# Kernel tuning notes

Hardware: AMD Instinct MI355X
Metric: run time of the kernel (lower is better)

The kernel has to match this reference:

```python
import jax, jax.numpy as jnp
import numpy as np

B, T, L, D, H, E, A, V = 64, 20, 196, 512, 512, 512, 512, 30000


def setup_inputs() -> dict:
    key = jax.random.key(0)
    ks = jax.random.split(key, 20)
    s = 0.02  # param init scale
    inp = {
        "captions": jax.random.randint(ks[0], (B, T), 0, V),
        "image_features": jax.random.normal(ks[1], (B, L, D), dtype=jnp.float32),
        "pooled_features": jax.random.normal(ks[2], (B, H), dtype=jnp.float32),
        "attention_mask": jnp.ones((B, L), dtype=bool),
        # embedding table
        "embedding": jax.random.normal(ks[3], (V, E), dtype=jnp.float32) * s,
        # LSTM (torch gate order i, f, g, o), input = [emb; context]
        "W_ih": jax.random.normal(ks[4], (4 * H, E + H), dtype=jnp.float32) * s,
        "W_hh": jax.random.normal(ks[5], (4 * H, H), dtype=jnp.float32) * s,
        "b_lstm": jnp.zeros((4 * H,), dtype=jnp.float32),
        # additive attention with memory/cell extra query context
        "Wq": jax.random.normal(ks[6], (H, A), dtype=jnp.float32) * s,
        "Wk": jax.random.normal(ks[7], (D, A), dtype=jnp.float32) * s,
        "Wm": jax.random.normal(ks[8], (H, A), dtype=jnp.float32) * s,
        "Wc": jax.random.normal(ks[9], (H, A), dtype=jnp.float32) * s,
        "v_att": jax.random.normal(ks[10], (A,), dtype=jnp.float32) * s,
        # output projection context(H) -> vocab
        "W_out": jax.random.normal(ks[11], (H, V), dtype=jnp.float32) * s,
        "b_out": jnp.zeros((V,), dtype=jnp.float32),
        # hidden/cell init from pooled features (num_layers = 1)
        "W_init_h": jax.random.normal(ks[12], (H, H), dtype=jnp.float32) * s,
        "b_init_h": jnp.zeros((H,), dtype=jnp.float32),
        "W_init_c": jax.random.normal(ks[13], (H, H), dtype=jnp.float32) * s,
        "b_init_c": jnp.zeros((H,), dtype=jnp.float32),
    }
    return inp


def reference(captions, image_features, pooled_features, attention_mask,
              embedding, W_ih, W_hh, b_lstm, Wq, Wk, Wm, Wc, v_att,
              W_out, b_out, W_init_h, b_init_h, W_init_c, b_init_c):
    # init hidden states from pooled features
    h0 = pooled_features @ W_init_h + b_init_h            # [B, H]
    c0 = pooled_features @ W_init_c + b_init_c            # [B, H]
    ctx0 = jnp.zeros_like(h0)                              # prev_context, [B, H]
    emb = embedding[captions]                              # [B, T, E] (dropout = eval identity)
    # precompute key projection once (hoisted out of the timestep loop)
    key_proj = jnp.einsum('bld,da->bla', image_features, Wk)  # [B, L, A]
    neg = jnp.finfo(image_features.dtype).min

    def step(carry, emb_t):
        h, c, ctx = carry
        x = jnp.concatenate([emb_t, ctx], axis=-1)         # [B, E+H]
        gates = x @ W_ih.T + h @ W_hh.T + b_lstm           # [B, 4H]
        i, f, g, o = jnp.split(gates, 4, axis=-1)
        i = jax.nn.sigmoid(i); f = jax.nn.sigmoid(f)
        g = jnp.tanh(g);       o = jax.nn.sigmoid(o)
        c_new = f * c + i * g
        h_new = o * jnp.tanh(c_new)                        # lstm output == query
        # additive attention: query + memory_state(h) + cell_state(c) context
        q = h_new @ Wq + h_new @ Wm + c_new @ Wc           # [B, A]
        scores = jnp.einsum('bla,a->bl', jnp.tanh(key_proj + q[:, None, :]), v_att)
        scores = jnp.where(attention_mask, scores, neg)
        w = jax.nn.softmax(scores, axis=-1)                # [B, L]
        ctx_new = jnp.einsum('bl,bld->bd', w, image_features)  # [B, H]
        logits_t = ctx_new @ W_out + b_out                 # [B, V]
        return (h_new, c_new, ctx_new), logits_t

    _, logits = jax.lax.scan(step, (h0, c0, ctx0), jnp.swapaxes(emb, 0, 1))
    return jnp.swapaxes(logits, 0, 1)  # [B, T, V]
```

## Files before the change

kernel.cpp:

```cpp
#include <hip/hip_runtime.h>
#include <hip/hip_bf16.h>
#include <cstdint>

#define DEV static __device__ __forceinline__

typedef __bf16 bf16;
typedef __bf16 bf16x8 __attribute__((ext_vector_type(8)));
typedef float f32x4 __attribute__((ext_vector_type(4)));

#define B_ 64
#define T_ 20
#define L_ 196
#define E_ 512
#define V_ 30000
#define VPAD 30080
#define XK 2560
#define GN 2048
#define KSPLIT 8
#define KSPAN 10

DEV float sigmoidf_(float x) { return 1.0f / (1.0f + __expf(-x)); }
DEV float tanhf_(float x) { float e = __expf(2.0f * x); return 1.0f - 2.0f / (e + 1.0f); }

DEV float ldf(const void* p, size_t i, int isbf) {
  return isbf ? (float)((const bf16*)p)[i] : ((const float*)p)[i];
}

DEV void gload_lds16(const void* g, void* l) {
  __builtin_amdgcn_global_load_lds(
      (const __attribute__((address_space(1))) void*)(uintptr_t)g,
      (__attribute__((address_space(3))) void*)(uint32_t)(uintptr_t)l,
      16, 0, 0);
}

__global__ void k_detect(const void* __restrict__ emb, int* __restrict__ flag)
{
  if (threadIdx.x == 0) {
    const unsigned* w = (const unsigned*)emb;
    int cnt = 0;
    for (int i = 0; i < 256; ++i) {
      unsigned lo = w[i] & 0xFFFFu;
      unsigned e = (lo >> 7) & 0xFFu;
      if (e >= 100 && e <= 126) ++cnt;
    }
    *flag = (cnt >= 128) ? 1 : 0;
  }
}

__global__ __launch_bounds__(256)
void k_init_mm(const void* __restrict__ pooled, const void* __restrict__ W_init_h,
               const void* __restrict__ W_init_c, float* __restrict__ ipart,
               const int* __restrict__ flag)
{
  const int isbf = *flag;
  const int b = blockIdx.x, ks = blockIdx.y, mat = blockIdx.z;
  const void* W = mat ? W_init_c : W_init_h;
  const int tid = threadIdx.x;
  __shared__ float p_s[64];
  if (tid < 64) p_s[tid] = ldf(pooled, (size_t)b * 512 + ks * 64 + tid, isbf);
  __syncthreads();
  const int kb = ks * 64;
  float a0 = 0.0f, a1 = 0.0f;
#pragma unroll 8
  for (int k = 0; k < 64; ++k) {
    float p = p_s[k];
    a0 += p * ldf(W, (size_t)(kb + k) * 512 + tid, isbf);
    a1 += p * ldf(W, (size_t)(kb + k) * 512 + tid + 256, isbf);
  }
  float* o = ipart + (((size_t)mat * 8 + ks) * 64 + b) * 512;
  o[tid] = a0;
  o[tid + 256] = a1;
}

__global__ __launch_bounds__(256)
void k_pack(const float* __restrict__ ipart, const void* __restrict__ b_init_h,
            const void* __restrict__ b_init_c, const int* __restrict__ captions,
            const void* __restrict__ embedding, const void* __restrict__ Wq,
            const void* __restrict__ Wm, const void* __restrict__ Wc,
            bf16* __restrict__ xcomb, float* __restrict__ c_state,
            bf16* __restrict__ Wqm, bf16* __restrict__ Wcb,
            const int* __restrict__ flag)
{
  const int isbf = *flag;
  const int tid = threadIdx.x;
  if (blockIdx.x >= 96) {
    size_t base = (size_t)(blockIdx.x - 96) * 8192;
    for (int i = tid; i < 8192; i += 256)
      Wcb[base + i] = (bf16)ldf(Wc, base + i, isbf);
    return;
  }
  if (blockIdx.x >= 64) {
    size_t base = (size_t)(blockIdx.x - 64) * 8192;
    for (int i = tid; i < 8192; i += 256)
      Wqm[base + i] = (bf16)(ldf(Wq, base + i, isbf) + ldf(Wm, base + i, isbf));
    return;
  }
  const int b = blockIdx.x;
  {
    int cap = captions[b * T_];
    for (int i = tid; i < 512; i += 256) {
      xcomb[(size_t)b * XK + i] = (bf16)ldf(embedding, (size_t)cap * E_ + i, isbf);
      xcomb[(size_t)b * XK + 512 + i]  = (bf16)0.0f;
      xcomb[(size_t)b * XK + 1024 + i] = (bf16)0.0f;
    }
  }
#pragma unroll
  for (int jj = 0; jj < 2; ++jj) {
    int j = tid + jj * 256;
    float ah = ldf(b_init_h, j, isbf), ac = ldf(b_init_c, j, isbf);
#pragma unroll
    for (int ks = 0; ks < 8; ++ks) {
      ah += ipart[(((size_t)0 * 8 + ks) * 64 + b) * 512 + j];
      ac += ipart[(((size_t)1 * 8 + ks) * 64 + b) * 512 + j];
    }
    c_state[b * 512 + j] = ac;
    bf16 hh = (bf16)ah;
    xcomb[(size_t)b * XK + 1536 + j] = hh;
    xcomb[(size_t)b * XK + 2048 + j] = (bf16)(ah - (float)hh);
  }
}

__global__ __launch_bounds__(256)
void k_gemm(const void* __restrict__ A, const void* __restrict__ Bsrc,
            int N, int K, int kspan, int outmode, int amode, int btmode,
            float* __restrict__ outF, bf16* __restrict__ outB,
            void* __restrict__ outAny, const void* __restrict__ bias,
            const int* __restrict__ flag)
{
  const int isbf = *flag;
  const int tid  = threadIdx.x;
  const int lane = tid & 63, w = tid >> 6;
  const int n0 = blockIdx.x * 64;
  const int yt = blockIdx.y;
  const int m0 = (outmode == 1) ? 0 : yt * 64;
  const int kbase = (outmode == 1) ? yt * kspan * 32 : 0;

  __shared__ __align__(16) bf16 As[64 * 32];
  __shared__ __align__(16) bf16 Bs[64 * 32];

  f32x4 acc[2][2];
#pragma unroll
  for (int i = 0; i < 2; ++i)
#pragma unroll
    for (int j = 0; j < 2; ++j)
#pragma unroll
      for (int r = 0; r < 4; ++r) acc[i][j][r] = 0.0f;

  const int wm = (w & 1) * 32, wn = (w >> 1) * 32;
  const int sr = tid >> 2, sk = (tid & 3) * 8;
  const int fm = lane & 15, kq = (lane >> 4) * 8;
  const bool bvalid = (n0 + sr) < N;
  const int kk = tid >> 3, nn = (tid & 7) * 8;

  for (int ks = 0; ks < kspan; ++ks) {
    const size_t aidx = (size_t)(m0 + sr) * K + kbase + sk + ks * 32;
    bf16x8 av;
    if (amode == 0 || isbf) {
      av = *(const bf16x8*)((const bf16*)A + aidx);
    } else {
      const float* af = (const float*)A + aidx;
      float4 x0 = *(const float4*)af, x1 = *(const float4*)(af + 4);
      av[0] = (bf16)x0.x; av[1] = (bf16)x0.y; av[2] = (bf16)x0.z; av[3] = (bf16)x0.w;
      av[4] = (bf16)x1.x; av[5] = (bf16)x1.y; av[6] = (bf16)x1.z; av[7] = (bf16)x1.w;
    }

    if (btmode == 0) {
      bf16x8 bv;
#pragma unroll
      for (int i = 0; i < 8; ++i) bv[i] = (bf16)0.0f;
      if (bvalid)
        bv = *(const bf16x8*)((const bf16*)Bsrc + (size_t)(n0 + sr) * K + kbase + sk + ks * 32);
      __syncthreads();
      *(bf16x8*)(As + sr * 32 + sk) = av;
      *(bf16x8*)(Bs + sr * 32 + sk) = bv;
      __syncthreads();
    } else {
      float bl[8];
      const int krow = kbase + ks * 32 + kk;
#pragma unroll
      for (int i = 0; i < 8; ++i) {
        int n = n0 + nn + i;
        bl[i] = (n < N) ? ldf(Bsrc, (size_t)krow * N + n, isbf) : 0.0f;
      }
      __syncthreads();
      *(bf16x8*)(As + sr * 32 + sk) = av;
#pragma unroll
      for (int i = 0; i < 8; ++i) Bs[(nn + i) * 32 + kk] = (bf16)bl[i];
      __syncthreads();
    }

    bf16x8 a0 = *(const bf16x8*)(As + (wm + fm)      * 32 + kq);
    bf16x8 a1 = *(const bf16x8*)(As + (wm + 16 + fm) * 32 + kq);
    bf16x8 b0 = *(const bf16x8*)(Bs + (wn + fm)      * 32 + kq);
    bf16x8 b1 = *(const bf16x8*)(Bs + (wn + 16 + fm) * 32 + kq);
    acc[0][0] = __builtin_amdgcn_mfma_f32_16x16x32_bf16(a0, b0, acc[0][0], 0, 0, 0);
    acc[0][1] = __builtin_amdgcn_mfma_f32_16x16x32_bf16(a0, b1, acc[0][1], 0, 0, 0);
    acc[1][0] = __builtin_amdgcn_mfma_f32_16x16x32_bf16(a1, b0, acc[1][0], 0, 0, 0);
    acc[1][1] = __builtin_amdgcn_mfma_f32_16x16x32_bf16(a1, b1, acc[1][1], 0, 0, 0);
  }

  const int rbase = (lane >> 4) * 4;
  if (outmode == 1) {
    float* o = outF + (size_t)yt * 64 * N;
#pragma unroll
    for (int i = 0; i < 2; ++i)
#pragma unroll
      for (int j = 0; j < 2; ++j)
#pragma unroll
        for (int r = 0; r < 4; ++r) {
          int m = wm + i * 16 + rbase + r;
          int n = n0 + wn + j * 16 + fm;
          o[(size_t)m * N + n] = acc[i][j][r];
        }
  } else if (outmode == 0) {
#pragma unroll
    for (int i = 0; i < 2; ++i)
#pragma unroll
      for (int j = 0; j < 2; ++j) {
        int n = n0 + wn + j * 16 + fm;
        if (n < N) {
#pragma unroll
          for (int r = 0; r < 4; ++r) {
            int m = m0 + wm + i * 16 + rbase + r;
            outB[(size_t)m * N + n] = (bf16)acc[i][j][r];
          }
        }
      }
  } else {
#pragma unroll
    for (int i = 0; i < 2; ++i)
#pragma unroll
      for (int j = 0; j < 2; ++j) {
        int n = n0 + wn + j * 16 + fm;
        if (n < N) {
          float bb = bias ? ldf(bias, n, isbf) : 0.0f;
#pragma unroll
          for (int r = 0; r < 4; ++r) {
            int m = m0 + wm + i * 16 + rbase + r;
            float val = acc[i][j][r] + bb;
            if (isbf) ((bf16*)outAny)[(size_t)m * N + n] = (bf16)val;
            else      ((float*)outAny)[(size_t)m * N + n] = val;
          }
        }
      }
  }
}

__global__ __launch_bounds__(256)
void k_gemm128(const bf16* __restrict__ A, const bf16* __restrict__ BT,
               int N, int K,
               void* __restrict__ outAny, const void* __restrict__ bias,
               const int* __restrict__ flag)
{
  const int isbf = *flag;
  const int tid = threadIdx.x, lane = tid & 63, w = tid >> 6;

  const int NMT = (B_ * T_) / 128;
  const int nwg = (int)gridDim.x * (int)gridDim.y;
  const int wgid = (int)blockIdx.y * (int)gridDim.x + (int)blockIdx.x;
  const int xcd = wgid & 7, loc = wgid >> 3;
  const int qq = nwg >> 3, rr = nwg & 7;
  const int swz = (xcd < rr ? xcd * (qq + 1) : rr * (qq + 1) + (xcd - rr) * qq) + loc;
  const int n0 = (swz / NMT) * 128, m0 = (swz % NMT) * 128;

  __shared__ __align__(16) bf16 As[128 * 32];
  __shared__ __align__(16) bf16 Bs[128 * 32];

  f32x4 acc[4][4];
#pragma unroll
  for (int i = 0; i < 4; ++i)
#pragma unroll
    for (int j = 0; j < 4; ++j)
#pragma unroll
      for (int r = 0; r < 4; ++r) acc[i][j][r] = 0.0f;

  const int lr = lane >> 2;
  const int lk = (lane & 3) * 8;
  const int fm = lane & 15, kq = (lane >> 4) * 8;
  const int wm = (w & 1) * 64, wn = (w >> 1) * 64;
  const int li0 = w * 2, li1 = w * 2 + 1;

  const bf16* a0g = A  + (size_t)(m0 + li0 * 16 + lr) * K + lk;
  const bf16* a1g = A  + (size_t)(m0 + li1 * 16 + lr) * K + lk;
  const bf16* b0g = BT + (size_t)(n0 + li0 * 16 + lr) * K + lk;
  const bf16* b1g = BT + (size_t)(n0 + li1 * 16 + lr) * K + lk;

  const int kiters = K >> 5;
  for (int ks = 0; ks < kiters; ++ks) {
    const int k0 = ks * 32;
    gload_lds16(a0g + k0, As + li0 * 512);
    gload_lds16(a1g + k0, As + li1 * 512);
    gload_lds16(b0g + k0, Bs + li0 * 512);
    gload_lds16(b1g + k0, Bs + li1 * 512);
    __syncthreads();
    bf16x8 af[4], bf[4];
#pragma unroll
    for (int i = 0; i < 4; ++i) {
      af[i] = *(const bf16x8*)(As + (wm + i * 16 + fm) * 32 + kq);
      bf[i] = *(const bf16x8*)(Bs + (wn + i * 16 + fm) * 32 + kq);
    }
#pragma unroll
    for (int i = 0; i < 4; ++i)
#pragma unroll
      for (int j = 0; j < 4; ++j)
        acc[i][j] = __builtin_amdgcn_mfma_f32_16x16x32_bf16(af[i], bf[j], acc[i][j], 0, 0, 0);
    __syncthreads();
  }

  const int rbase = (lane >> 4) * 4;
#pragma unroll
  for (int j = 0; j < 4; ++j) {
    int n = n0 + wn + j * 16 + fm;
    if (n < N) {
      float bb = bias ? ldf(bias, n, isbf) : 0.0f;
#pragma unroll
      for (int i = 0; i < 4; ++i)
#pragma unroll
        for (int r = 0; r < 4; ++r) {
          int m = m0 + wm + i * 16 + rbase + r;
          float val = acc[i][j][r] + bb;
          if (isbf) ((bf16*)outAny)[(size_t)m * N + n] = (bf16)val;
          else      ((float*)outAny)[(size_t)m * N + n] = val;
        }
    }
  }
}

__global__ __launch_bounds__(256)
void k_transpose(const void* __restrict__ in, bf16* __restrict__ out, int R, int C,
                 int Cpad, const int* __restrict__ flag)
{
  const int isbf = *flag;
  __shared__ bf16 tile[32][33];
  const int c0 = blockIdx.x * 32, r0 = blockIdx.y * 32;
  const int cc = threadIdx.x & 31, rw = threadIdx.x >> 5;
#pragma unroll
  for (int s = 0; s < 4; ++s) {
    int r = r0 + rw + s * 8, c = c0 + cc;
    tile[rw + s * 8][cc] = (r < R && c < C) ? (bf16)ldf(in, (size_t)r * C + c, isbf)
                                            : (bf16)0.0f;
  }
  __syncthreads();
#pragma unroll
  for (int s = 0; s < 4; ++s) {
    int c = c0 + rw + s * 8, r = r0 + cc;
    if (c < Cpad && r < R) out[(size_t)c * R + r] = tile[cc][rw + s * 8];
  }
}

__global__ __launch_bounds__(256)
void k_buildWcomb(const void* __restrict__ W_ih, const void* __restrict__ W_hh,
                  bf16* __restrict__ WcombT, const int* __restrict__ flag)
{
  const int isbf = *flag;
  const int n = blockIdx.x;
  for (int k = threadIdx.x; k < XK; k += 256) {
    float v;
    if (k < 512)       v = ldf(W_ih, (size_t)n * 1024 + k, isbf);
    else if (k < 1536) v = ldf(W_ih, (size_t)n * 1024 + 512 + ((k - 512) & 511), isbf);
    else               v = ldf(W_hh, (size_t)n * 512 + ((k - 1536) & 511), isbf);
    WcombT[(size_t)n * XK + k] = (bf16)v;
  }
}

__global__ __launch_bounds__(1024)
void k_step2(const float* __restrict__ partials, const void* __restrict__ b_lstm,
             float* __restrict__ c_state, bf16* __restrict__ xcomb,
             bf16* __restrict__ ctx_all, const bf16* __restrict__ Wqm,
             const bf16* __restrict__ Wcb, const bf16* __restrict__ keyproj,
             const void* __restrict__ v_att, const void* __restrict__ img,
             const int* __restrict__ captions, const void* __restrict__ embedding,
             int t, const int* __restrict__ flag)
{
  const int isbf = *flag;
  const int b = blockIdx.x, tid = threadIdx.x;
  __shared__ float h_s[512], c_s[512], q_s[512];
  __shared__ float red[16 * 512];
  __shared__ float sc_s[256];
  __shared__ float wred[32];

#pragma unroll
  for (int jj = 0; jj < 2; ++jj) {
    int gc = tid + jj * 1024;
    float s = ldf(b_lstm, gc, isbf);
#pragma unroll
    for (int sp = 0; sp < KSPLIT; ++sp)
      s += partials[((size_t)sp * 64 + b) * 2048 + gc];
    red[gc] = s;
  }
  __syncthreads();
  if (tid < 512) {
    const int j = tid;
    float ig = sigmoidf_(red[j]);
    float fg = sigmoidf_(red[512 + j]);
    float gg = tanhf_(red[1024 + j]);
    float og = sigmoidf_(red[1536 + j]);
    float cn = fg * c_state[b * 512 + j] + ig * gg;
    float hn = og * tanhf_(cn);
    c_state[b * 512 + j] = cn;
    h_s[j] = hn; c_s[j] = cn;
    bf16 hh = (bf16)hn;
    xcomb[(size_t)b * XK + 1536 + j] = hh;
    xcomb[(size_t)b * XK + 2048 + j] = (bf16)(hn - (float)hh);
  }
  __syncthreads();

  {
    const int dc = tid >> 6, a8 = (tid & 63) * 8;
    float qp[8];
#pragma unroll
    for (int i = 0; i < 8; ++i) qp[i] = 0.0f;
    const int d0 = dc * 32;
    for (int d = d0; d < d0 + 32; ++d) {
      float hv = h_s[d], cv = c_s[d];
      bf16x8 wq = *(const bf16x8*)(Wqm + (size_t)d * 512 + a8);
      bf16x8 wc = *(const bf16x8*)(Wcb + (size_t)d * 512 + a8);
#pragma unroll
      for (int i = 0; i < 8; ++i)
        qp[i] += hv * (float)wq[i] + cv * (float)wc[i];
    }
#pragma unroll
    for (int i = 0; i < 8; ++i) red[dc * 512 + a8 + i] = qp[i];
  }
  __syncthreads();
  if (tid < 512) {
    float s = 0.0f;
#pragma unroll
    for (int w16 = 0; w16 < 16; ++w16) s += red[w16 * 512 + tid];
    q_s[tid] = s;
  }
  __syncthreads();

  {
    const int wv = tid >> 6, ln = tid & 63;
    float q8[8], v8[8];
#pragma unroll
    for (int i = 0; i < 8; ++i) {
      q8[i] = q_s[ln * 8 + i];
      v8[i] = ldf(v_att, ln * 8 + i, isbf);
    }
    for (int l = wv; l < 196; l += 16) {
      bf16x8 kv = *(const bf16x8*)(keyproj + ((size_t)b * 196 + l) * 512 + ln * 8);
      float s = 0.0f;
#pragma unroll
      for (int i = 0; i < 8; ++i)
        s += tanhf_((float)kv[i] + q8[i]) * v8[i];
      s += __shfl_xor(s, 32); s += __shfl_xor(s, 16); s += __shfl_xor(s, 8);
      s += __shfl_xor(s, 4);  s += __shfl_xor(s, 2);  s += __shfl_xor(s, 1);
      if (ln == 0) sc_s[l] = s;
    }
  }
  __syncthreads();

  {
    const int wv = tid >> 6, ln = tid & 63;
    float v = (tid < 196) ? sc_s[tid] : -3.0e38f;
    float m = v;
    m = fmaxf(m, __shfl_xor(m, 32)); m = fmaxf(m, __shfl_xor(m, 16));
    m = fmaxf(m, __shfl_xor(m, 8));  m = fmaxf(m, __shfl_xor(m, 4));
    m = fmaxf(m, __shfl_xor(m, 2));  m = fmaxf(m, __shfl_xor(m, 1));
    if (ln == 0) wred[wv] = m;
    __syncthreads();
    m = wred[0];
#pragma unroll
    for (int i = 1; i < 16; ++i) m = fmaxf(m, wred[i]);
    float e = (tid < 196) ? __expf(v - m) : 0.0f;
    float ss = e;
    ss += __shfl_xor(ss, 32); ss += __shfl_xor(ss, 16); ss += __shfl_xor(ss, 8);
    ss += __shfl_xor(ss, 4);  ss += __shfl_xor(ss, 2);  ss += __shfl_xor(ss, 1);
    if (ln == 0) wred[16 + wv] = ss;
    __syncthreads();
    float tot = 0.0f;
#pragma unroll
    for (int i = 0; i < 16; ++i) tot += wred[16 + i];
    if (tid < 196) sc_s[tid] = e / tot;
  }
  __syncthreads();

  {
    const int d8 = (tid & 63) * 8, lc = tid >> 6;
    float cx[8];
#pragma unroll
    for (int i = 0; i < 8; ++i) cx[i] = 0.0f;
    if (isbf) {
      for (int l = lc; l < 196; l += 16) {
        float wl = sc_s[l];
        bf16x8 iv = *(const bf16x8*)((const bf16*)img + ((size_t)b * 196 + l) * 512 + d8);
#pragma unroll
        for (int i = 0; i < 8; ++i) cx[i] += wl * (float)iv[i];
      }
    } else {
      for (int l = lc; l < 196; l += 16) {
        float wl = sc_s[l];
        const float* ip = (const float*)img + ((size_t)b * 196 + l) * 512 + d8;
        float4 x0 = *(const float4*)ip, x1 = *(const float4*)(ip + 4);
        cx[0] += wl * x0.x; cx[1] += wl * x0.y; cx[2] += wl * x0.z; cx[3] += wl * x0.w;
        cx[4] += wl * x1.x; cx[5] += wl * x1.y; cx[6] += wl * x1.z; cx[7] += wl * x1.w;
      }
    }
#pragma unroll
    for (int i = 0; i < 8; ++i) red[lc * 512 + d8 + i] = cx[i];
  }
  __syncthreads();
  if (tid < 512) {
    const int d = tid;
    float s = 0.0f;
#pragma unroll
    for (int w16 = 0; w16 < 16; ++w16) s += red[w16 * 512 + d];
    bf16 ch = (bf16)s;
    xcomb[(size_t)b * XK + 512 + d]  = ch;
    xcomb[(size_t)b * XK + 1024 + d] = (bf16)(s - (float)ch);
    ctx_all[((size_t)b * T_ + t) * 512 + d] = ch;
  }
  if (t + 1 < T_) {
    int cap = captions[b * T_ + t + 1];
    for (int i = tid; i < 512; i += 1024)
      xcomb[(size_t)b * XK + i] = (bf16)ldf(embedding, (size_t)cap * E_ + i, isbf);
  }
}

extern "C" void kernel_launch(void* const* d_in, const int* in_sizes, int n_in,
                              void* d_out, int out_size, void* d_ws, size_t ws_size,
                              hipStream_t stream)
{
  (void)in_sizes; (void)n_in; (void)out_size;
  const int*  captions  = (const int*)d_in[0];
  const void* img       = d_in[1];
  const void* pooled    = d_in[2];
  const void* embedding = d_in[4];
  const void* W_ih      = d_in[5];
  const void* W_hh      = d_in[6];
  const void* b_lstm    = d_in[7];
  const void* Wq        = d_in[8];
  const void* Wk        = d_in[9];
  const void* Wm        = d_in[10];
  const void* Wc        = d_in[11];
  const void* v_att     = d_in[12];
  const void* W_out     = d_in[13];
  const void* b_out     = d_in[14];
  const void* W_init_h  = d_in[15];
  const void* b_init_h  = d_in[16];
  const void* W_init_c  = d_in[17];
  const void* b_init_c  = d_in[18];

  char* ws = (char*)d_ws;
  size_t off = 0;
  auto alloc = [&](size_t bytes) {
    void* p = ws + off;
    off += (bytes + 255) & ~(size_t)255;
    return p;
  };
  int*   flag     = (int*)alloc(256);
  bf16*  xcomb    = (bf16*)alloc((size_t)B_ * XK * 2);
  float* c_state  = (float*)alloc((size_t)B_ * 512 * 4);
  bf16*  ctx_all  = (bf16*)alloc((size_t)B_ * T_ * 512 * 2);
  bf16*  Wqm      = (bf16*)alloc((size_t)512 * 512 * 2);
  bf16*  Wcb      = (bf16*)alloc((size_t)512 * 512 * 2);
  bf16*  WkT      = (bf16*)alloc((size_t)512 * 512 * 2);
  float* partials = (float*)alloc((size_t)KSPLIT * B_ * GN * 4);
  bf16*  keyproj  = (bf16*)alloc((size_t)B_ * L_ * 512 * 2);
  bf16*  WcombT   = (bf16*)alloc((size_t)GN * XK * 2);
  bf16*  WoutT    = (bf16*)alloc((size_t)VPAD * 512 * 2);
  const bool fits = (off <= ws_size);
  float* ipart = partials;

  k_detect<<<1, 64, 0, stream>>>(embedding, flag);
  k_init_mm<<<dim3(64, 8, 2), 256, 0, stream>>>(pooled, W_init_h, W_init_c, ipart, flag);
  k_pack<<<128, 256, 0, stream>>>(ipart, b_init_h, b_init_c, captions, embedding,
                                  Wq, Wm, Wc, xcomb, c_state, Wqm, Wcb, flag);
  k_buildWcomb<<<GN, 256, 0, stream>>>(W_ih, W_hh, WcombT, flag);
  k_transpose<<<dim3(16, 16), 256, 0, stream>>>(Wk, WkT, 512, 512, 512, flag);
  if (fits)
    k_transpose<<<dim3(VPAD / 32, 16), 256, 0, stream>>>(W_out, WoutT, 512, V_, VPAD, flag);

  k_gemm<<<dim3(8, L_ * B_ / 64), 256, 0, stream>>>(
      img, WkT, 512, 512, 16, 0, 1, 0,
      nullptr, keyproj, nullptr, nullptr, flag);

  for (int t = 0; t < T_; ++t) {
    k_gemm<<<dim3(GN / 64, KSPLIT), 256, 0, stream>>>(
        xcomb, WcombT, GN, XK, KSPAN, 1, 0, 0,
        partials, nullptr, nullptr, nullptr, flag);
    k_step2<<<B_, 1024, 0, stream>>>(partials, b_lstm, c_state, xcomb, ctx_all,
                                     Wqm, Wcb, keyproj, v_att, img, captions,
                                     embedding, t, flag);
  }

  if (fits) {
    k_gemm128<<<dim3(VPAD / 128, B_ * T_ / 128), 256, 0, stream>>>(
        ctx_all, WoutT, V_, 512, d_out, b_out, flag);
  } else {
    k_gemm<<<dim3((V_ + 63) / 64, B_ * T_ / 64), 256, 0, stream>>>(
        ctx_all, W_out, V_, 512, 16, 2, 0, 1,
        nullptr, nullptr, d_out, b_out, flag);
  }
}
```

Measured before the change: 1.393 ms.

## Double-buffer LDS loads in gate and vocab GEMMs with a dedicated gates kernel

Adds a specialized k_gates kernel for the per-step LSTM gate GEMM. It double-buffers global-to-LDS loads and uses manual vmcnt waits and barriers, so the next K-slice is fetched while MFMAs run on the current one. k_gemm128 (the vocab projection) gets the same two-stage LDS pipeline, which doubles its shared-memory use. The aim is to hide global load latency in these short-K GEMMs. The cost is hand-written waitcnt logic and higher LDS pressure, which could reduce occupancy.

```diff
diff --git a/kernel.cpp b/kernel.cpp
--- a/kernel.cpp
+++ b/kernel.cpp
@@ -33,6 +33,14 @@
       16, 0, 0);
 }
 
+#define WAITV4_BAR  do { asm volatile("s_waitcnt vmcnt(4)" ::: "memory"); \
+                         asm volatile("s_barrier" ::: "memory"); } while (0)
+#define WAITV2_BAR  do { asm volatile("s_waitcnt vmcnt(2)" ::: "memory"); \
+                         asm volatile("s_barrier" ::: "memory"); } while (0)
+#define WAITV0_BAR  do { asm volatile("s_waitcnt vmcnt(0)" ::: "memory"); \
+                         asm volatile("s_barrier" ::: "memory"); } while (0)
+#define BAR_ONLY    do { asm volatile("s_barrier" ::: "memory"); } while (0)
+
 __global__ void k_detect(const void* __restrict__ emb, int* __restrict__ flag)
 {
   if (threadIdx.x == 0) {
@@ -247,6 +255,70 @@
 }
 
 __global__ __launch_bounds__(256)
+void k_gates(const bf16* __restrict__ A, const bf16* __restrict__ BT,
+             float* __restrict__ outF)
+{
+  const int tid = threadIdx.x, lane = tid & 63, w = tid >> 6;
+  const int n0 = blockIdx.x * 64;
+  const int yt = blockIdx.y;
+  const int kbase = yt * KSPAN * 32;
+
+  __shared__ __align__(16) bf16 As[2][64 * 32];
+  __shared__ __align__(16) bf16 Bs[2][64 * 32];
+
+  f32x4 acc[2][2];
+#pragma unroll
+  for (int i = 0; i < 2; ++i)
+#pragma unroll
+    for (int j = 0; j < 2; ++j)
+#pragma unroll
+      for (int r = 0; r < 4; ++r) acc[i][j][r] = 0.0f;
+
+  const int wm = (w & 1) * 32, wn = (w >> 1) * 32;
+  const int fm = lane & 15, kq = (lane >> 4) * 8;
+
+  const int srow = w * 16 + (lane >> 2), skk = (lane & 3) * 8;
+  const bf16* ag = A  + (size_t)srow * XK + kbase + skk;
+  const bf16* bg = BT + (size_t)(n0 + srow) * XK + kbase + skk;
+
+#define GSTAGE(cur, koff) do { \
+    gload_lds16(ag + (koff), &As[cur][w * 512]); \
+    gload_lds16(bg + (koff), &Bs[cur][w * 512]); } while (0)
+
+  GSTAGE(0, 0);
+  GSTAGE(1, 32);
+  int cur = 0;
+  for (int ks = 0; ks < KSPAN; ++ks) {
+    if (ks + 1 < KSPAN) WAITV2_BAR; else WAITV0_BAR;
+    bf16x8 a0 = *(const bf16x8*)(&As[cur][(wm + fm)      * 32 + kq]);
+    bf16x8 a1 = *(const bf16x8*)(&As[cur][(wm + 16 + fm) * 32 + kq]);
+    bf16x8 b0 = *(const bf16x8*)(&Bs[cur][(wn + fm)      * 32 + kq]);
+    bf16x8 b1 = *(const bf16x8*)(&Bs[cur][(wn + 16 + fm) * 32 + kq]);
+    acc[0][0] = __builtin_amdgcn_mfma_f32_16x16x32_bf16(a0, b0, acc[0][0], 0, 0, 0);
+    acc[0][1] = __builtin_amdgcn_mfma_f32_16x16x32_bf16(a0, b1, acc[0][1], 0, 0, 0);
+    acc[1][0] = __builtin_amdgcn_mfma_f32_16x16x32_bf16(a1, b0, acc[1][0], 0, 0, 0);
+    acc[1][1] = __builtin_amdgcn_mfma_f32_16x16x32_bf16(a1, b1, acc[1][1], 0, 0, 0);
+    BAR_ONLY;
+    if (ks + 2 < KSPAN) GSTAGE(cur, (ks + 2) * 32);
+    cur ^= 1;
+  }
+#undef GSTAGE
+
+  const int rbase = (lane >> 4) * 4;
+  float* o = outF + (size_t)yt * 64 * GN;
+#pragma unroll
+  for (int i = 0; i < 2; ++i)
+#pragma unroll
+    for (int j = 0; j < 2; ++j)
+#pragma unroll
+      for (int r = 0; r < 4; ++r) {
+        int m = wm + i * 16 + rbase + r;
+        int n = n0 + wn + j * 16 + fm;
+        o[(size_t)m * GN + n] = acc[i][j][r];
+      }
+}
+
+__global__ __launch_bounds__(256)
 void k_gemm128(const bf16* __restrict__ A, const bf16* __restrict__ BT,
                int N, int K,
                void* __restrict__ outAny, const void* __restrict__ bias,
@@ -263,8 +335,8 @@
   const int swz = (xcd < rr ? xcd * (qq + 1) : rr * (qq + 1) + (xcd - rr) * qq) + loc;
   const int n0 = (swz / NMT) * 128, m0 = (swz % NMT) * 128;
 
-  __shared__ __align__(16) bf16 As[128 * 32];
-  __shared__ __align__(16) bf16 Bs[128 * 32];
+  __shared__ __align__(16) bf16 As[2][128 * 32];
+  __shared__ __align__(16) bf16 Bs[2][128 * 32];
 
   f32x4 acc[4][4];
 #pragma unroll
@@ -285,27 +357,34 @@
   const bf16* b0g = BT + (size_t)(n0 + li0 * 16 + lr) * K + lk;
   const bf16* b1g = BT + (size_t)(n0 + li1 * 16 + lr) * K + lk;
 
+#define STAGE128(cur, koff) do { \
+    gload_lds16(a0g + (koff), &As[cur][li0 * 512]); \
+    gload_lds16(a1g + (koff), &As[cur][li1 * 512]); \
+    gload_lds16(b0g + (koff), &Bs[cur][li0 * 512]); \
+    gload_lds16(b1g + (koff), &Bs[cur][li1 * 512]); } while (0)
+
   const int kiters = K >> 5;
+  STAGE128(0, 0);
+  STAGE128(1, 32);
+  int cur = 0;
   for (int ks = 0; ks < kiters; ++ks) {
-    const int k0 = ks * 32;
-    gload_lds16(a0g + k0, As + li0 * 512);
-    gload_lds16(a1g + k0, As + li1 * 512);
-    gload_lds16(b0g + k0, Bs + li0 * 512);
-    gload_lds16(b1g + k0, Bs + li1 * 512);
-    __syncthreads();
+    if (ks + 1 < kiters) WAITV4_BAR; else WAITV0_BAR;
     bf16x8 af[4], bf[4];
 #pragma unroll
     for (int i = 0; i < 4; ++i) {
-      af[i] = *(const bf16x8*)(As + (wm + i * 16 + fm) * 32 + kq);
-      bf[i] = *(const bf16x8*)(Bs + (wn + i * 16 + fm) * 32 + kq);
+      af[i] = *(const bf16x8*)(&As[cur][(wm + i * 16 + fm) * 32 + kq]);
+      bf[i] = *(const bf16x8*)(&Bs[cur][(wn + i * 16 + fm) * 32 + kq]);
     }
 #pragma unroll
     for (int i = 0; i < 4; ++i)
 #pragma unroll
       for (int j = 0; j < 4; ++j)
         acc[i][j] = __builtin_amdgcn_mfma_f32_16x16x32_bf16(af[i], bf[j], acc[i][j], 0, 0, 0);
-    __syncthreads();
-  }
+    BAR_ONLY;
+    if (ks + 2 < kiters) STAGE128(cur, (ks + 2) * 32);
+    cur ^= 1;
+  }
+#undef STAGE128
 
   const int rbase = (lane >> 4) * 4;
 #pragma unroll
@@ -578,9 +657,7 @@
       nullptr, keyproj, nullptr, nullptr, flag);
 
   for (int t = 0; t < T_; ++t) {
-    k_gemm<<<dim3(GN / 64, KSPLIT), 256, 0, stream>>>(
-        xcomb, WcombT, GN, XK, KSPAN, 1, 0, 0,
-        partials, nullptr, nullptr, nullptr, flag);
+    k_gates<<<dim3(GN / 64, KSPLIT), 256, 0, stream>>>(xcomb, WcombT, partials);
     k_step2<<<B_, 1024, 0, stream>>>(partials, b_lstm, c_state, xcomb, ctx_all,
                                      Wqm, Wcb, keyproj, v_att, img, captions,
                                      embedding, t, flag);
```

Result: faster. 1.347 ms (-3.3%).
